# Kernel optimization log

Measured on AMD Instinct MI355X. Metric: run time of the kernel, lower is better.

## Reference

```python
import jax, jax.numpy as jnp
import numpy as np

N = 20000      # total nodes across the mini-batch of graphs
E = 320000     # edges (avg degree 16)
B = 16         # graphs in the batch
HEADS = 8
EPS_BN = 1e-5
NEG_SLOPE = 0.2


def _lin(k, fan_in, fan_out):
    return (jax.random.normal(k, (fan_in, fan_out), jnp.float32) / np.float32(np.sqrt(fan_in)))


def setup_inputs() -> dict:
    key = jax.random.key(0)
    ks = jax.random.split(key, 24)
    inp = {}
    inp["x"] = jax.random.normal(ks[0], (N, 3), jnp.float32)
    inp["edge_index"] = jax.random.randint(ks[1], (2, E), 0, N, dtype=jnp.int32)
    inp["batch"] = jnp.sort(jax.random.randint(ks[2], (N,), 0, B, dtype=jnp.int32))
    # GATConv params: lin weight [in, heads*out], att_src/att_dst [heads,out], bias [heads*out]
    dims = [(3, 16), (128, 32), (256, 64)]
    for i, (cin, cout) in enumerate(dims, start=1):
        base = 3 + 5 * i
        inp[f"W{i}"] = _lin(ks[base], cin, HEADS * cout)
        inp[f"as{i}"] = jax.random.normal(ks[base + 1], (HEADS, cout), jnp.float32) * 0.1
        inp[f"ad{i}"] = jax.random.normal(ks[base + 2], (HEADS, cout), jnp.float32) * 0.1
        inp[f"b{i}"] = jnp.zeros((HEADS * cout,), jnp.float32)
        inp[f"g{i}"] = jnp.ones((HEADS * cout,), jnp.float32)
        inp[f"be{i}"] = jnp.zeros((HEADS * cout,), jnp.float32)
    inp["fcW"] = _lin(ks[20], 512, 10)
    inp["fcb"] = jnp.zeros((10,), jnp.float32)
    return inp


def gat_layer(x, src, dst, W, a_s, a_d, bias, heads, out_ch):
    n = x.shape[0]
    h = (x @ W).reshape(n, heads, out_ch)              # [N,H,C]
    al_s = jnp.einsum('nhc,hc->nh', h, a_s)            # [N,H]
    al_d = jnp.einsum('nhc,hc->nh', h, a_d)
    e = jax.nn.leaky_relu(al_s[src] + al_d[dst], NEG_SLOPE)   # [E,H]
    m = jax.ops.segment_max(e, dst, num_segments=n)    # per-dst softmax (stable)
    e = jnp.exp(e - m[dst])
    denom = jax.ops.segment_sum(e, dst, num_segments=n)
    alpha = e / (denom[dst] + 1e-16)
    out = jax.ops.segment_sum(h[src] * alpha[:, :, None], dst, num_segments=n)
    return out.reshape(n, heads * out_ch) + bias


def bn_relu(x, g, b):
    mu = x.mean(0)
    var = x.var(0)  # biased, as torch BN uses for normalization
    return jax.nn.relu((x - mu) * jax.lax.rsqrt(var + EPS_BN) * g + b)


def reference(x, edge_index, batch, W1, as1, ad1, b1, g1, be1,
              W2, as2, ad2, b2, g2, be2, W3, as3, ad3, b3, g3, be3, fcW, fcb):
    n = x.shape[0]
    loops = jnp.arange(n, dtype=edge_index.dtype)
    src = jnp.concatenate([edge_index[0], loops])  # add_self_loops=True (PyG default)
    dst = jnp.concatenate([edge_index[1], loops])
    h = bn_relu(gat_layer(x, src, dst, W1, as1, ad1, b1, HEADS, 16), g1, be1)
    h = bn_relu(gat_layer(h, src, dst, W2, as2, ad2, b2, HEADS, 32), g2, be2)
    h = bn_relu(gat_layer(h, src, dst, W3, as3, ad3, b3, HEADS, 64), g3, be3)
    pooled = jax.ops.segment_max(h, batch, num_segments=B)  # global_max_pool
    return pooled @ fcW + fcb
```

## Files before the change

kernel.cpp:

```cpp
#include <hip/hip_runtime.h>
#include <hip/hip_bf16.h>

#define HEADS 8
#define EPS_BN 1e-5f
#define NEG_SLOPE 0.2f
#define BN_NB 256

typedef __attribute__((ext_vector_type(8))) short bf16x8;
typedef __attribute__((ext_vector_type(4))) float f32x4;

__device__ __forceinline__ float bf2f(unsigned short u) {
    return __uint_as_float(((unsigned int)u) << 16);
}

__device__ __forceinline__ unsigned short f2bf(float f) {
    __hip_bfloat16 b = __float2bfloat16(f);
    return *reinterpret_cast<unsigned short*>(&b);
}

__device__ __forceinline__ void gld_lds16(const ushort* g, ushort* l) {
    __builtin_amdgcn_global_load_lds(
        (const __attribute__((address_space(1))) unsigned int*)g,
        (__attribute__((address_space(3))) unsigned int*)l, 16, 0, 0);
}


__global__ void count_kernel(const int* __restrict__ ei, int E, int N, int* __restrict__ counts) {
    int i = blockIdx.x * blockDim.x + threadIdx.x;
    int total = E + N;
    if (i >= total) return;
    int d = (i < E) ? ei[E + i] : (i - E);
    atomicAdd(&counts[d], 1);
}

__global__ __launch_bounds__(1024) void scan_block_kernel(const int* __restrict__ counts,
                                                          int* __restrict__ offs,
                                                          int* __restrict__ part, int n) {
    __shared__ int tile[1024];
    int tid = threadIdx.x;
    int gid = blockIdx.x * 1024 + tid;
    int v = (gid < n) ? counts[gid] : 0;
    tile[tid] = v;
    __syncthreads();
    for (int off = 1; off < 1024; off <<= 1) {
        int t = (tid >= off) ? tile[tid - off] : 0;
        __syncthreads();
        tile[tid] += t;
        __syncthreads();
    }
    if (gid < n) offs[gid + 1] = tile[tid];
    if (tid == 1023) part[blockIdx.x] = tile[1023];
}

__global__ __launch_bounds__(1024) void scan_add_kernel(int* __restrict__ offs,
                                                        const int* __restrict__ part, int n) {
    __shared__ int base;
    if (threadIdx.x == 0) {
        int s = 0;
        for (int i = 0; i < (int)blockIdx.x; ++i) s += part[i];
        base = s;
    }
    __syncthreads();
    int gid = blockIdx.x * 1024 + threadIdx.x;
    if (gid < n) offs[gid + 1] += base;
    if (gid == 0) offs[0] = 0;
}

__global__ void scatter_kernel(const int* __restrict__ ei, int E, int N,
                               const int* __restrict__ offs, int* __restrict__ cursor,
                               int* __restrict__ csr_src) {
    int i = blockIdx.x * blockDim.x + threadIdx.x;
    int total = E + N;
    if (i >= total) return;
    int s, d;
    if (i < E) { s = ei[i]; d = ei[E + i]; } else { s = i - E; d = i - E; }
    int slot = atomicAdd(&cursor[d], 1);
    csr_src[offs[d] + slot] = s;
}


__global__ __launch_bounds__(256) void linear1_al_kernel(const float* __restrict__ x,
                                                         const float* __restrict__ W,
                                                         const float* __restrict__ a_s,
                                                         const float* __restrict__ a_d,
                                                         ushort* __restrict__ h,
                                                         float* __restrict__ als,
                                                         float* __restrict__ ald, int N) {
    int tid = threadIdx.x;
    int n = blockIdx.x * 2 + (tid >> 7);
    int f = tid & 127;
    if (n >= N) return;
    float acc = x[n * 3 + 0] * W[f] + x[n * 3 + 1] * W[128 + f] + x[n * 3 + 2] * W[256 + f];
    h[(size_t)n * 128 + f] = f2bf(acc);
    float s = acc * a_s[f];
    float ds = acc * a_d[f];
    s += __shfl_xor(s, 1);  ds += __shfl_xor(ds, 1);
    s += __shfl_xor(s, 2);  ds += __shfl_xor(ds, 2);
    s += __shfl_xor(s, 4);  ds += __shfl_xor(ds, 4);
    s += __shfl_xor(s, 8);  ds += __shfl_xor(ds, 8);
    if ((f & 15) == 0) {
        int head = f >> 4;
        als[n * 8 + head] = s;
        ald[n * 8 + head] = ds;
    }
}


__global__ __launch_bounds__(256) void transpose_both_kernel(const float* __restrict__ W2,
                                                             ushort* __restrict__ Wt2,
                                                             const float* __restrict__ W3,
                                                             ushort* __restrict__ Wt3) {
    __shared__ float t[32][33];
    int bid = blockIdx.x;
    const float* W; ushort* Wt; int K, Nc, b;
    if (bid < 32) { W = W2; Wt = Wt2; K = 128; Nc = 256; b = bid; }
    else          { W = W3; Wt = Wt3; K = 256; Nc = 512; b = bid - 32; }
    int nb = Nc / 32;
    int bx = b % nb, by = b / nb;
    int n0 = bx * 32, k0 = by * 32;
    int lx = threadIdx.x & 31, ly = threadIdx.x >> 5;
    for (int r = ly; r < 32; r += 8) t[r][lx] = W[(size_t)(k0 + r) * Nc + n0 + lx];
    __syncthreads();
    for (int r = ly; r < 32; r += 8) Wt[(size_t)(n0 + r) * K + k0 + lx] = f2bf(t[lx][r]);
}


template<int F>
__global__ void prep_kernel(const float4* __restrict__ x, const float* __restrict__ scale,
                            const float* __restrict__ shift, ushort4* __restrict__ A, int n4) {
    int i = blockIdx.x * blockDim.x + threadIdx.x;
    if (i >= n4) return;
    float4 v = x[i];
    int f = (i << 2) & (F - 1);
    float4 sc = *(const float4*)(scale + f);
    float4 sh = *(const float4*)(shift + f);
    ushort4 u;
    u.x = f2bf(fmaxf(v.x * sc.x + sh.x, 0.f));
    u.y = f2bf(fmaxf(v.y * sc.y + sh.y, 0.f));
    u.z = f2bf(fmaxf(v.z * sc.z + sh.z, 0.f));
    u.w = f2bf(fmaxf(v.w * sc.w + sh.w, 0.f));
    A[i] = u;
}


template<int K, int C>
__global__ __launch_bounds__(256) void mfma_gemm_kernel(const ushort* __restrict__ A,
                                                        const ushort* __restrict__ Bt,
                                                        ushort* __restrict__ Cout,
                                                        const float* __restrict__ a_s,
                                                        const float* __restrict__ a_d,
                                                        float* __restrict__ als,
                                                        float* __restrict__ ald,
                                                        int M, int Ncols) {
    __shared__ __align__(16) ushort lA[128 * 64];
    __shared__ __align__(16) ushort lB[128 * 64];
    int tid = threadIdx.x;
    int l = tid & 63, w = tid >> 6;
    int m0 = blockIdx.x * 128;
    int n0 = blockIdx.y * 128;
    int wm = w >> 1, wn = w & 1;
    f32x4 zero = {0.f, 0.f, 0.f, 0.f};
    f32x4 acc[4][4];
#pragma unroll
    for (int m = 0; m < 4; ++m)
#pragma unroll
        for (int n = 0; n < 4; ++n) acc[m][n] = zero;

#pragma unroll
    for (int k0 = 0; k0 < K; k0 += 64) {
        if (k0) __syncthreads();
#pragma unroll
        for (int i = 0; i < 4; ++i) {
            int idx = (w * 4 + i) * 64 + l;
            int row = idx >> 3, p = idx & 7;
            int gc = (p ^ (row & 7)) * 8;
            int ar = m0 + row; ar = (ar < M) ? ar : (M - 1);
            gld_lds16(A + (size_t)ar * K + k0 + gc, &lA[idx * 8]);
            gld_lds16(Bt + (size_t)(n0 + row) * K + k0 + gc, &lB[idx * 8]);
        }
        __syncthreads();
#pragma unroll
        for (int ks = 0; ks < 2; ++ks) {
            bf16x8 af[4], bfr[4];
#pragma unroll
            for (int m = 0; m < 4; ++m) {
                int row = wm * 64 + m * 16 + (l & 15);
                int cp = (ks * 4 + (l >> 4)) ^ (row & 7);
                af[m] = *(const bf16x8*)&lA[row * 64 + cp * 8];
            }
#pragma unroll
            for (int n = 0; n < 4; ++n) {
                int row = wn * 64 + n * 16 + (l & 15);
                int cp = (ks * 4 + (l >> 4)) ^ (row & 7);
                bfr[n] = *(const bf16x8*)&lB[row * 64 + cp * 8];
            }
#pragma unroll
            for (int m = 0; m < 4; ++m)
#pragma unroll
                for (int n = 0; n < 4; ++n)
                    acc[m][n] = __builtin_amdgcn_mfma_f32_16x16x32_bf16(af[m], bfr[n], acc[m][n], 0, 0, 0);
        }
    }
    int lr = (l >> 4) * 4, lc = l & 15;
#pragma unroll
    for (int m = 0; m < 4; ++m) {
#pragma unroll
        for (int q = 0; q < 4; ++q) {
            int r = m0 + wm * 64 + m * 16 + lr + q;
            if (r < M) {
#pragma unroll
                for (int n = 0; n < 4; ++n) {
                    int c = n0 + wn * 64 + n * 16 + lc;
                    Cout[(size_t)r * Ncols + c] = f2bf(acc[m][n][q]);
                }
            }
        }
    }
    constexpr int GRP = (C == 64) ? 4 : 2;
    constexpr int NGRP = 4 / GRP;
    float asv[4], adv[4];
#pragma unroll
    for (int n = 0; n < 4; ++n) {
        int cc = n0 + wn * 64 + n * 16 + lc;
        asv[n] = a_s[cc];
        adv[n] = a_d[cc];
    }
#pragma unroll
    for (int m = 0; m < 4; ++m) {
#pragma unroll
        for (int q = 0; q < 4; ++q) {
            int r = m0 + wm * 64 + m * 16 + lr + q;
#pragma unroll
            for (int gg = 0; gg < NGRP; ++gg) {
                float s = 0.f, ds = 0.f;
#pragma unroll
                for (int nn = 0; nn < GRP; ++nn) {
                    int n = gg * GRP + nn;
                    s += acc[m][n][q] * asv[n];
                    ds += acc[m][n][q] * adv[n];
                }
                s += __shfl_xor(s, 1);  ds += __shfl_xor(ds, 1);
                s += __shfl_xor(s, 2);  ds += __shfl_xor(ds, 2);
                s += __shfl_xor(s, 4);  ds += __shfl_xor(ds, 4);
                s += __shfl_xor(s, 8);  ds += __shfl_xor(ds, 8);
                if (lc == 0 && r < M) {
                    int head = (n0 + wn * 64 + gg * (GRP * 16)) / C;
                    als[r * 8 + head] = s;
                    ald[r * 8 + head] = ds;
                }
            }
        }
    }
}


template<int CPL>
__device__ __forceinline__ void gather_accum(const ushort* hp, float wt, float* acc) {
    unsigned int u[CPL / 2];
    if constexpr (CPL == 8) {
        uint4 v = *(const uint4*)hp; u[0] = v.x; u[1] = v.y; u[2] = v.z; u[3] = v.w;
    } else if constexpr (CPL == 4) {
        uint2 v = *(const uint2*)hp; u[0] = v.x; u[1] = v.y;
    } else {
        u[0] = *(const unsigned int*)hp;
    }
#pragma unroll
    for (int j = 0; j < CPL / 2; ++j) {
        acc[2 * j]     += wt * __uint_as_float(u[j] << 16);
        acc[2 * j + 1] += wt * __uint_as_float(u[j] & 0xffff0000u);
    }
}

template<int F, int C>
__global__ __launch_bounds__(256) void aggregate_kernel(const ushort* __restrict__ h,
                                                        const float* __restrict__ als,
                                                        const float* __restrict__ ald,
                                                        const int* __restrict__ offs,
                                                        const int* __restrict__ csr_src,
                                                        const float* __restrict__ bias,
                                                        float* __restrict__ out, int N) {
    constexpr int CPL = F / 64;
    int w = threadIdx.x >> 6, l = threadIdx.x & 63;
    int d = blockIdx.x * 4 + w;
    if (d >= N) return;
    int start = offs[d];
    int deg = offs[d + 1] - start;
    int hf = l >> 3;
    int sub = l & 7;
    float aldv = ald[d * 8 + hf];

    float m = -1e30f;
    for (int e = sub; e < deg; e += 8) {
        int s = csr_src[start + e];
        float v = als[s * 8 + hf] + aldv;
        v = (v > 0.f) ? v : NEG_SLOPE * v;
        m = fmaxf(m, v);
    }
    m = fmaxf(m, __shfl_xor(m, 1));
    m = fmaxf(m, __shfl_xor(m, 2));
    m = fmaxf(m, __shfl_xor(m, 4));
    float den = 0.f;
    for (int e = sub; e < deg; e += 8) {
        int s = csr_src[start + e];
        float v = als[s * 8 + hf] + aldv;
        v = (v > 0.f) ? v : NEG_SLOPE * v;
        den += __expf(v - m);
    }
    den += __shfl_xor(den, 1);
    den += __shfl_xor(den, 2);
    den += __shfl_xor(den, 4);

    float acc[CPL];
#pragma unroll
    for (int j = 0; j < CPL; ++j) acc[j] = 0.f;
    int e = 0;
    for (; e + 2 <= deg; e += 2) {
        int s0 = csr_src[start + e];
        int s1 = csr_src[start + e + 1];
        float v0 = als[s0 * 8 + hf] + aldv;
        float v1 = als[s1 * 8 + hf] + aldv;
        v0 = (v0 > 0.f) ? v0 : NEG_SLOPE * v0;
        v1 = (v1 > 0.f) ? v1 : NEG_SLOPE * v1;
        float w0 = __expf(v0 - m);
        float w1 = __expf(v1 - m);
        gather_accum<CPL>(h + (size_t)s0 * F + l * CPL, w0, acc);
        gather_accum<CPL>(h + (size_t)s1 * F + l * CPL, w1, acc);
    }
    if (e < deg) {
        int s0 = csr_src[start + e];
        float v0 = als[s0 * 8 + hf] + aldv;
        v0 = (v0 > 0.f) ? v0 : NEG_SLOPE * v0;
        gather_accum<CPL>(h + (size_t)s0 * F + l * CPL, __expf(v0 - m), acc);
    }

    float inv = 1.0f / (den + 1e-16f);
    int cbase = l * CPL;
#pragma unroll
    for (int j = 0; j < CPL; ++j)
        out[(size_t)d * F + cbase + j] = acc[j] * inv + bias[cbase + j];
}


template<int F>
__global__ __launch_bounds__(256) void bnA_kernel(const float4* __restrict__ x4,
                                                  float* __restrict__ part,
                                                  int N, int npb) {
    constexpr int F4 = F / 4;
    constexpr int RPI = 256 / F4;
    __shared__ float sdata[256 * 8];
    int tid = threadIdx.x;
    int c4 = tid % F4;
    int ro = tid / F4;
    int n0 = blockIdx.x * npb;
    int n1 = n0 + npb;
    if (n1 > N) n1 = N;
    float s0 = 0, s1 = 0, s2 = 0, s3 = 0, q0 = 0, q1 = 0, q2 = 0, q3 = 0;
    for (int r = n0 + ro; r < n1; r += RPI) {
        float4 v = x4[(size_t)r * F4 + c4];
        s0 += v.x; s1 += v.y; s2 += v.z; s3 += v.w;
        q0 += v.x * v.x; q1 += v.y * v.y; q2 += v.z * v.z; q3 += v.w * v.w;
    }
    float* sp = &sdata[tid * 8];
    sp[0] = s0; sp[1] = s1; sp[2] = s2; sp[3] = s3;
    sp[4] = q0; sp[5] = q1; sp[6] = q2; sp[7] = q3;
    __syncthreads();
    if (tid < F4) {
        float t[8];
#pragma unroll
        for (int k = 0; k < 8; ++k) t[k] = sdata[tid * 8 + k];
        for (int j = 1; j < RPI; ++j) {
            const float* op = &sdata[(j * F4 + tid) * 8];
#pragma unroll
            for (int k = 0; k < 8; ++k) t[k] += op[k];
        }
        float* pb = part + (size_t)blockIdx.x * 2 * F;
#pragma unroll
        for (int k = 0; k < 4; ++k) {
            pb[tid * 4 + k]     = t[k];
            pb[F + tid * 4 + k] = t[4 + k];
        }
    }
}

template<int F>
__global__ void bnB_kernel(const float* __restrict__ part,
                           const float* __restrict__ g, const float* __restrict__ be,
                           float* __restrict__ scale, float* __restrict__ shift, int N) {
    int f = blockIdx.x * blockDim.x + threadIdx.x;
    if (f >= F) return;
    float sum = 0.f, sq = 0.f;
#pragma unroll 4
    for (int j = 0; j < BN_NB; ++j) {
        sum += part[(size_t)j * 2 * F + f];
        sq  += part[(size_t)j * 2 * F + F + f];
    }
    float invN = 1.0f / (float)N;
    float mean = sum * invN;
    float var = sq * invN - mean * mean;
    float sc = g[f] * rsqrtf(var + EPS_BN);
    scale[f] = sc;
    shift[f] = be[f] - mean * sc;
}


__global__ __launch_bounds__(256) void poolA_kernel(const float4* __restrict__ x4,
                                                    const int* __restrict__ batch,
                                                    const float* __restrict__ scale,
                                                    const float* __restrict__ shift,
                                                    float* __restrict__ pooled8, int N) {
    int tid = threadIdx.x;
    int c4 = tid & 127;
    int ro = tid >> 7;
    int n0 = blockIdx.x * 64;
    int n1 = n0 + 64;
    if (n1 > N) n1 = N;
    float4 sc = ((const float4*)scale)[c4];
    float4 sh = ((const float4*)shift)[c4];
    float* pbase = pooled8 + (size_t)(blockIdx.x & 7) * (16 * 512);
    float m0 = 0.f, m1 = 0.f, m2 = 0.f, m3 = 0.f;
    int cur = -1;
    for (int n = n0 + ro; n < n1; n += 2) {
        int b = batch[n];
        if (b != cur) {
            if (cur >= 0) {
                int base = cur * 512 + c4 * 4;
                atomicMax((int*)&pbase[base],     __float_as_int(m0));
                atomicMax((int*)&pbase[base + 1], __float_as_int(m1));
                atomicMax((int*)&pbase[base + 2], __float_as_int(m2));
                atomicMax((int*)&pbase[base + 3], __float_as_int(m3));
            }
            cur = b;
            m0 = m1 = m2 = m3 = 0.f;
        }
        float4 v = x4[(size_t)n * 128 + c4];
        m0 = fmaxf(m0, v.x * sc.x + sh.x);
        m1 = fmaxf(m1, v.y * sc.y + sh.y);
        m2 = fmaxf(m2, v.z * sc.z + sh.z);
        m3 = fmaxf(m3, v.w * sc.w + sh.w);
    }
    if (cur >= 0) {
        int base = cur * 512 + c4 * 4;
        atomicMax((int*)&pbase[base],     __float_as_int(m0));
        atomicMax((int*)&pbase[base + 1], __float_as_int(m1));
        atomicMax((int*)&pbase[base + 2], __float_as_int(m2));
        atomicMax((int*)&pbase[base + 3], __float_as_int(m3));
    }
}

__global__ __launch_bounds__(512) void poolFC_kernel(const float* __restrict__ pooled8,
                                                     const float* __restrict__ fcW,
                                                     const float* __restrict__ fcb,
                                                     float* __restrict__ out) {
    __shared__ float sp[16 * 513];
    __shared__ float sw[512 * 10];
    int tid = threadIdx.x;
    for (int c = tid; c < 16 * 512; c += 512) {
        float m = pooled8[c];
#pragma unroll
        for (int k = 1; k < 8; ++k) m = fmaxf(m, pooled8[k * 16 * 512 + c]);
        int b = c >> 9, f = c & 511;
        sp[b * 513 + f] = m;
    }
    for (int i = tid; i < 512 * 10; i += 512) sw[i] = fcW[i];
    __syncthreads();
    if (tid < 160) {
        int b = tid / 10, j = tid % 10;
        float acc = fcb[j];
        const float* spb = &sp[b * 513];
#pragma unroll 8
        for (int f = 0; f < 512; ++f) acc += spb[f] * sw[f * 10 + j];
        out[tid] = acc;
    }
}


extern "C" void kernel_launch(void* const* d_in, const int* in_sizes, int n_in,
                              void* d_out, int out_size, void* d_ws, size_t ws_size,
                              hipStream_t stream) {
    const float* x   = (const float*)d_in[0];
    const int* ei    = (const int*)d_in[1];
    const int* batch = (const int*)d_in[2];
    const float* W1  = (const float*)d_in[3];
    const float* as1 = (const float*)d_in[4];
    const float* ad1 = (const float*)d_in[5];
    const float* b1  = (const float*)d_in[6];
    const float* g1  = (const float*)d_in[7];
    const float* be1 = (const float*)d_in[8];
    const float* W2  = (const float*)d_in[9];
    const float* as2 = (const float*)d_in[10];
    const float* ad2 = (const float*)d_in[11];
    const float* b2  = (const float*)d_in[12];
    const float* g2  = (const float*)d_in[13];
    const float* be2 = (const float*)d_in[14];
    const float* W3  = (const float*)d_in[15];
    const float* as3 = (const float*)d_in[16];
    const float* ad3 = (const float*)d_in[17];
    const float* b3  = (const float*)d_in[18];
    const float* g3  = (const float*)d_in[19];
    const float* be3 = (const float*)d_in[20];
    const float* fcW = (const float*)d_in[21];
    const float* fcb = (const float*)d_in[22];
    float* out = (float*)d_out;

    int N = in_sizes[0] / 3;
    int E = in_sizes[1] / 2;

    char* p = (char*)d_ws;
    auto alloc = [&](size_t bytes) {
        char* r = p;
        p += (bytes + 255) & ~(size_t)255;
        return r;
    };
    char* zbase   = p;
    int*   counts = (int*)alloc((size_t)N * 4);
    int*   cursor = (int*)alloc((size_t)N * 4);
    float* pooled8 = (float*)alloc(8 * 16 * 512 * 4);
    size_t zbytes = (size_t)(p - zbase);
    int*   offs   = (int*)alloc((size_t)(N + 1) * 4);
    int*   part   = (int*)alloc(64 * 4);
    int*   csr    = (int*)alloc((size_t)(E + N) * 4);
    ushort* h     = (ushort*)alloc((size_t)N * 512 * 2);
    float* agg    = (float*)alloc((size_t)N * 512 * 4);
    ushort* Wt2   = (ushort*)alloc(256 * 128 * 2);
    ushort* Wt3   = (ushort*)alloc(512 * 256 * 2);
    float* als    = (float*)alloc((size_t)N * 8 * 4);
    float* ald    = (float*)alloc((size_t)N * 8 * 4);
    float* bnpart = (float*)alloc((size_t)BN_NB * 1024 * 4);
    float* scale  = (float*)alloc(512 * 4);
    float* shift  = (float*)alloc(512 * 4);
    ushort* Abuf  = (ushort*)(agg + (size_t)N * 256);

    int total_e = E + N;
    int nchunks = (N + 1023) / 1024;
    int mtiles = (N + 127) / 128;
    int bnnpb = (N + BN_NB - 1) / BN_NB;
    int ablocks = (N + 3) / 4;
    int pblocks = (N + 63) / 64;

    hipMemsetAsync(zbase, 0, zbytes, stream);

    count_kernel<<<(total_e + 255) / 256, 256, 0, stream>>>(ei, E, N, counts);
    scan_block_kernel<<<nchunks, 1024, 0, stream>>>(counts, offs, part, N);
    scan_add_kernel<<<nchunks, 1024, 0, stream>>>(offs, part, N);
    scatter_kernel<<<(total_e + 255) / 256, 256, 0, stream>>>(ei, E, N, offs, cursor, csr);

    transpose_both_kernel<<<160, 256, 0, stream>>>(W2, Wt2, W3, Wt3);

    linear1_al_kernel<<<(N + 1) / 2, 256, 0, stream>>>(x, W1, as1, ad1, h, als, ald, N);
    aggregate_kernel<128, 16><<<ablocks, 256, 0, stream>>>(h, als, ald, offs, csr, b1, agg, N);
    bnA_kernel<128><<<BN_NB, 256, 0, stream>>>((const float4*)agg, bnpart, N, bnnpb);
    bnB_kernel<128><<<1, 128, 0, stream>>>(bnpart, g1, be1, scale, shift, N);

    prep_kernel<128><<<(N * 128 / 4 + 255) / 256, 256, 0, stream>>>(
        (const float4*)agg, scale, shift, (ushort4*)Abuf, N * 128 / 4);
    mfma_gemm_kernel<128, 32><<<dim3(mtiles, 2), 256, 0, stream>>>(
        Abuf, Wt2, h, as2, ad2, als, ald, N, 256);
    aggregate_kernel<256, 32><<<ablocks, 256, 0, stream>>>(h, als, ald, offs, csr, b2, agg, N);
    bnA_kernel<256><<<BN_NB, 256, 0, stream>>>((const float4*)agg, bnpart, N, bnnpb);
    bnB_kernel<256><<<1, 256, 0, stream>>>(bnpart, g2, be2, scale, shift, N);

    prep_kernel<256><<<(N * 256 / 4 + 255) / 256, 256, 0, stream>>>(
        (const float4*)agg, scale, shift, (ushort4*)Abuf, N * 256 / 4);
    mfma_gemm_kernel<256, 64><<<dim3(mtiles, 4), 256, 0, stream>>>(
        Abuf, Wt3, h, as3, ad3, als, ald, N, 512);
    aggregate_kernel<512, 64><<<ablocks, 256, 0, stream>>>(h, als, ald, offs, csr, b3, agg, N);
    bnA_kernel<512><<<BN_NB, 256, 0, stream>>>((const float4*)agg, bnpart, N, bnnpb);
    bnB_kernel<512><<<2, 256, 0, stream>>>(bnpart, g3, be3, scale, shift, N);

    poolA_kernel<<<pblocks, 256, 0, stream>>>((const float4*)agg, batch, scale, shift, pooled8, N);
    poolFC_kernel<<<1, 512, 0, stream>>>(pooled8, fcW, fcb, out);
}
```

Before: 362.4 us.

## Fuse softmax denominator into gather loop and share edge weights via shuffles

Measured after the change: 338.2 us. -6.7%, faster.

```diff
diff --git a/kernel.cpp b/kernel.cpp
--- a/kernel.cpp
+++ b/kernel.cpp
@@ -286,53 +286,65 @@
     int start = offs[d];
     int deg = offs[d + 1] - start;
     int hf = l >> 3;
-    int sub = l & 7;
-    float aldv = ald[d * 8 + hf];
+    int hw = l & 7;
+    int jslot = l >> 3;
+    float aldw = ald[d * 8 + hw];
 
     float m = -1e30f;
-    for (int e = sub; e < deg; e += 8) {
-        int s = csr_src[start + e];
-        float v = als[s * 8 + hf] + aldv;
+    for (int eb = 0; eb < deg; eb += 8) {
+        int sE = 0;
+        if (l < 8 && eb + l < deg) sE = csr_src[start + eb + l];
+        int sj = __shfl(sE, jslot);
+        if (eb + jslot < deg) {
+            float v = als[sj * 8 + hw] + aldw;
+            v = (v > 0.f) ? v : NEG_SLOPE * v;
+            m = fmaxf(m, v);
+        }
+    }
+    m = fmaxf(m, __shfl_xor(m, 8));
+    m = fmaxf(m, __shfl_xor(m, 16));
+    m = fmaxf(m, __shfl_xor(m, 32));
+
+    float acc[CPL];
+#pragma unroll
+    for (int j = 0; j < CPL; ++j) acc[j] = 0.f;
+    float dsum = 0.f;
+    int nfull = deg & ~7;
+    for (int eb = 0; eb < nfull; eb += 8) {
+        int sE = (l < 8) ? csr_src[start + eb + l] : 0;
+        int smy = __shfl(sE, jslot);
+        float v = als[smy * 8 + hw] + aldw;
         v = (v > 0.f) ? v : NEG_SLOPE * v;
-        m = fmaxf(m, v);
-    }
-    m = fmaxf(m, __shfl_xor(m, 1));
-    m = fmaxf(m, __shfl_xor(m, 2));
-    m = fmaxf(m, __shfl_xor(m, 4));
-    float den = 0.f;
-    for (int e = sub; e < deg; e += 8) {
-        int s = csr_src[start + e];
-        float v = als[s * 8 + hf] + aldv;
-        v = (v > 0.f) ? v : NEG_SLOPE * v;
-        den += __expf(v - m);
-    }
-    den += __shfl_xor(den, 1);
-    den += __shfl_xor(den, 2);
-    den += __shfl_xor(den, 4);
-
-    float acc[CPL];
-#pragma unroll
-    for (int j = 0; j < CPL; ++j) acc[j] = 0.f;
-    int e = 0;
-    for (; e + 2 <= deg; e += 2) {
-        int s0 = csr_src[start + e];
-        int s1 = csr_src[start + e + 1];
-        float v0 = als[s0 * 8 + hf] + aldv;
-        float v1 = als[s1 * 8 + hf] + aldv;
-        v0 = (v0 > 0.f) ? v0 : NEG_SLOPE * v0;
-        v1 = (v1 > 0.f) ? v1 : NEG_SLOPE * v1;
-        float w0 = __expf(v0 - m);
-        float w1 = __expf(v1 - m);
-        gather_accum<CPL>(h + (size_t)s0 * F + l * CPL, w0, acc);
-        gather_accum<CPL>(h + (size_t)s1 * F + l * CPL, w1, acc);
-    }
-    if (e < deg) {
-        int s0 = csr_src[start + e];
-        float v0 = als[s0 * 8 + hf] + aldv;
-        v0 = (v0 > 0.f) ? v0 : NEG_SLOPE * v0;
-        gather_accum<CPL>(h + (size_t)s0 * F + l * CPL, __expf(v0 - m), acc);
-    }
-
+        float pw = __expf(v - m);
+        dsum += pw;
+#pragma unroll
+        for (int j = 0; j < 8; ++j) {
+            int sj = __shfl(sE, j);
+            float wt = __shfl(pw, (j << 3) + hf);
+            gather_accum<CPL>(h + (size_t)sj * F + l * CPL, wt, acc);
+        }
+    }
+    int rem = deg - nfull;
+    if (rem) {
+        int sE = (l < rem) ? csr_src[start + nfull + l] : 0;
+        int smy = __shfl(sE, jslot);
+        float pw = 0.f;
+        if (jslot < rem) {
+            float v = als[smy * 8 + hw] + aldw;
+            v = (v > 0.f) ? v : NEG_SLOPE * v;
+            pw = __expf(v - m);
+        }
+        dsum += pw;
+        for (int j = 0; j < rem; ++j) {
+            int sj = __shfl(sE, j);
+            float wt = __shfl(pw, (j << 3) + hf);
+            gather_accum<CPL>(h + (size_t)sj * F + l * CPL, wt, acc);
+        }
+    }
+    dsum += __shfl_xor(dsum, 8);
+    dsum += __shfl_xor(dsum, 16);
+    dsum += __shfl_xor(dsum, 32);
+    float den = __shfl(dsum, hf);
     float inv = 1.0f / (den + 1e-16f);
     int cbase = l * CPL;
 #pragma unroll
```
